# Performance work log

Hardware: AMD Instinct MI355X
Metric: run time of the kernel (lower is better)

## Reference

```python
import jax, jax.numpy as jnp
import numpy as np
from jax import lax

KH = KW = 3
PAD = 1
GROUPS = 3


def setup_inputs() -> dict:
    key = jax.random.key(0)
    k1, k2 = jax.random.split(key)
    x = jax.random.normal(k1, (16, 3, 1024, 1024), dtype=jnp.float32)
    weight = jax.random.normal(k2, (3, 1, KH, KW), dtype=jnp.float32)
    return {"x": x, "weight": weight}


def _norm_conv(x, weight):
    # Normalize each output-channel filter by its L2 norm over the 3x3 window
    w_norm = weight / jnp.linalg.norm(weight.reshape(3, KH * KW), axis=-1).reshape(3, 1, 1, 1)
    xp = jnp.pad(x, ((0, 0), (0, 0), (PAD, PAD), (PAD, PAD)))
    dn = ("NCHW", "OIHW", "NCHW")
    # numerator: depthwise correlation of x with normalized weights
    # (x_patch / ||x_patch||) . w_norm == (x_patch . w_norm) / ||x_patch||
    num = lax.conv_general_dilated(xp, w_norm, (1, 1), "VALID",
                                   dimension_numbers=dn,
                                   feature_group_count=GROUPS)
    ones = jnp.ones((3, 1, KH, KW), x.dtype)
    sq = lax.conv_general_dilated(xp * xp, ones, (1, 1), "VALID",
                                  dimension_numbers=dn,
                                  feature_group_count=GROUPS)
    patch_norm = jnp.sqrt(sq)  # per-(n,c) L2 norm of each 3x3 patch
    return num / patch_norm


def reference(x, weight):
    return _norm_conv(x, weight)
```

## Files before the change

### kernel.cpp

```cpp
#include <hip/hip_runtime.h>


#define HH 1024
#define WW 1024
#define CC 3
#define NN 16

__global__ __launch_bounds__(256) void normconv_kernel(
    const float* __restrict__ x, const float* __restrict__ w, float* __restrict__ out)
{
    const int row   = blockIdx.x & (HH - 1);
    const int plane = blockIdx.x >> 10;
    const int c     = plane % CC;

    float wn[9];
    float s = 0.f;
#pragma unroll
    for (int i = 0; i < 9; ++i) { float wi = w[c * 9 + i]; wn[i] = wi; s += wi * wi; }
    const float winv = rsqrtf(s);
#pragma unroll
    for (int i = 0; i < 9; ++i) wn[i] *= winv;

    const int x0 = threadIdx.x << 2;
    const float* base = x + (size_t)plane * (HH * WW);

    float v[3][6];
#pragma unroll
    for (int r = 0; r < 3; ++r) {
        const int y = row + r - 1;
        if (y < 0 || y >= HH) {
#pragma unroll
            for (int k = 0; k < 6; ++k) v[r][k] = 0.f;
        } else {
            const float* p = base + y * WW;
            const float4 c4 = *(const float4*)(p + x0);
            v[r][0] = (x0 > 0)        ? p[x0 - 1] : 0.f;
            v[r][1] = c4.x; v[r][2] = c4.y; v[r][3] = c4.z; v[r][4] = c4.w;
            v[r][5] = (x0 + 4 < WW)   ? p[x0 + 4] : 0.f;
        }
    }

    float4 o;
    float* op = &o.x;
#pragma unroll
    for (int j = 0; j < 4; ++j) {
        float num = 0.f, sq = 0.f;
#pragma unroll
        for (int r = 0; r < 3; ++r)
#pragma unroll
            for (int k = 0; k < 3; ++k) {
                const float val = v[r][j + k];
                num += val * wn[r * 3 + k];
                sq  += val * val;
            }
        op[j] = num * rsqrtf(sq);
    }

    *(float4*)(out + (size_t)plane * (HH * WW) + (size_t)row * WW + x0) = o;
}

extern "C" void kernel_launch(void* const* d_in, const int* in_sizes, int n_in,
                              void* d_out, int out_size, void* d_ws, size_t ws_size,
                              hipStream_t stream) {
    const float* x = (const float*)d_in[0];
    const float* w = (const float*)d_in[1];
    float* out = (float*)d_out;

    const int blocks = NN * CC * HH;
    normconv_kernel<<<blocks, 256, 0, stream>>>(x, w, out);
}
```

Before: 365.6 us.

## Process eight rows per block with rolling register window and XCD-aware block remap

```diff
diff --git a/kernel.cpp b/kernel.cpp
--- a/kernel.cpp
+++ b/kernel.cpp
@@ -5,12 +5,32 @@
 #define WW 1024
 #define CC 3
 #define NN 16
+#define ROWS 8
+#define TILES (HH / ROWS)
+#define NBLK (NN * CC * TILES)
+
+__device__ __forceinline__ void load_row(const float* __restrict__ base, int y,
+                                         int x0, float* __restrict__ dst)
+{
+    if ((unsigned)y >= (unsigned)HH) {
+#pragma unroll
+        for (int k = 0; k < 6; ++k) dst[k] = 0.f;
+    } else {
+        const float* p = base + y * WW;
+        const float4 c4 = *(const float4*)(p + x0);
+        dst[0] = (x0 > 0)      ? p[x0 - 1] : 0.f;
+        dst[1] = c4.x; dst[2] = c4.y; dst[3] = c4.z; dst[4] = c4.w;
+        dst[5] = (x0 + 4 < WW) ? p[x0 + 4] : 0.f;
+    }
+}
 
 __global__ __launch_bounds__(256) void normconv_kernel(
     const float* __restrict__ x, const float* __restrict__ w, float* __restrict__ out)
 {
-    const int row   = blockIdx.x & (HH - 1);
-    const int plane = blockIdx.x >> 10;
+    const int b     = blockIdx.x;
+    const int L     = (b & 7) * (NBLK / 8) + (b >> 3);
+    const int tile  = L & (TILES - 1);
+    const int plane = L >> 7;
     const int c     = plane % CC;
 
     float wn[9];
@@ -22,41 +42,37 @@
     for (int i = 0; i < 9; ++i) wn[i] *= winv;
 
     const int x0 = threadIdx.x << 2;
-    const float* base = x + (size_t)plane * (HH * WW);
+    const int y0 = tile * ROWS;
+    const float* base  = x   + (size_t)plane * (HH * WW);
+    float*       obase = out + (size_t)plane * (HH * WW);
 
     float v[3][6];
+    load_row(base, y0 - 1, x0, v[0]);
+    load_row(base, y0,     x0, v[1]);
+
 #pragma unroll
-    for (int r = 0; r < 3; ++r) {
-        const int y = row + r - 1;
-        if (y < 0 || y >= HH) {
+    for (int i = 0; i < ROWS; ++i) {
+        const int y = y0 + i;
+        load_row(base, y + 1, x0, v[(i + 2) % 3]);
+        const float* r0 = v[(i + 0) % 3];
+        const float* r1 = v[(i + 1) % 3];
+        const float* r2 = v[(i + 2) % 3];
+
+        float4 o;
+        float* op = &o.x;
 #pragma unroll
-            for (int k = 0; k < 6; ++k) v[r][k] = 0.f;
-        } else {
-            const float* p = base + y * WW;
-            const float4 c4 = *(const float4*)(p + x0);
-            v[r][0] = (x0 > 0)        ? p[x0 - 1] : 0.f;
-            v[r][1] = c4.x; v[r][2] = c4.y; v[r][3] = c4.z; v[r][4] = c4.w;
-            v[r][5] = (x0 + 4 < WW)   ? p[x0 + 4] : 0.f;
-        }
-    }
-
-    float4 o;
-    float* op = &o.x;
-#pragma unroll
-    for (int j = 0; j < 4; ++j) {
-        float num = 0.f, sq = 0.f;
-#pragma unroll
-        for (int r = 0; r < 3; ++r)
+        for (int j = 0; j < 4; ++j) {
+            float num = 0.f, sq = 0.f;
 #pragma unroll
             for (int k = 0; k < 3; ++k) {
-                const float val = v[r][j + k];
-                num += val * wn[r * 3 + k];
-                sq  += val * val;
+                const float a0 = r0[j + k], a1 = r1[j + k], a2 = r2[j + k];
+                num += a0 * wn[k] + a1 * wn[3 + k] + a2 * wn[6 + k];
+                sq  += a0 * a0 + a1 * a1 + a2 * a2;
             }
-        op[j] = num * rsqrtf(sq);
+            op[j] = num * rsqrtf(sq);
+        }
+        *(float4*)(obase + (size_t)y * WW + x0) = o;
     }
-
-    *(float4*)(out + (size_t)plane * (HH * WW) + (size_t)row * WW + x0) = o;
 }
 
 extern "C" void kernel_launch(void* const* d_in, const int* in_sizes, int n_in,
@@ -66,6 +82,5 @@
     const float* w = (const float*)d_in[1];
     float* out = (float*)d_out;
 
-    const int blocks = NN * CC * HH;
-    normconv_kernel<<<blocks, 256, 0, stream>>>(x, w, out);
+    normconv_kernel<<<NBLK, 256, 0, stream>>>(x, w, out);
 }
```

Result: faster. 344.3 us (-5.8%).
